# Kernel optimization log

Measured on AMD Instinct MI355X. Metric: run time of the kernel, lower is better.

Reference implementation:

```python
import jax, jax.numpy as jnp
import numpy as np

SIZES = jnp.array([128.0, 256.0, 512.0], dtype=jnp.float32)
RATIOS = jnp.array([0.5, 1.0, 2.0], dtype=jnp.float32)
SCORE_THR = 0.05
IOU_THR = 0.7
MIN_SIZE = 16.0
MAX_PROP = 1000
PRE_NMS = 1000


def _base_anchors():
    # torchvision-style base anchors: (x1,y1,x2,y2) centered at origin, rounded
    h_r = jnp.sqrt(RATIOS)
    w_r = 1.0 / h_r
    ws = (w_r[:, None] * SIZES[None, :]).reshape(-1)  # (9,)
    hs = (h_r[:, None] * SIZES[None, :]).reshape(-1)
    return jnp.round(jnp.stack([-ws, -hs, ws, hs], axis=1) / 2.0)  # (9,4)


def _grid_anchors(img_h, img_w, fh, fw):
    # stride = image_size // feature_size; anchors ordered (y, x, anchor)
    sh, sw = img_h // fh, img_w // fw
    sx = jnp.arange(fw, dtype=jnp.float32) * sw
    sy = jnp.arange(fh, dtype=jnp.float32) * sh
    yy, xx = jnp.meshgrid(sy, sx, indexing='ij')
    xf = xx.reshape(-1)
    yf = yy.reshape(-1)
    shifts = jnp.stack([xf, yf, xf, yf], axis=1)  # (H*W, 4)
    return (shifts[:, None, :] + _base_anchors()[None, :, :]).reshape(-1, 4)  # (H*W*9, 4)


def _conv(x, w, b, pad):
    y = jax.lax.conv_general_dilated(x, w, (1, 1), pad,
                                     dimension_numbers=('NCHW', 'OIHW', 'NCHW'))
    return y + b[None, :, None, None]


def _bbox_adjust(anchors, deltas):
    # anchors, deltas: (..., 4); deltas = (dx, dy, dw, dh)
    aw = anchors[..., 2] - anchors[..., 0]
    ah = anchors[..., 3] - anchors[..., 1]
    cx = anchors[..., 0] + 0.5 * aw
    cy = anchors[..., 1] + 0.5 * ah
    ncx = deltas[..., 0] * aw + cx
    ncy = deltas[..., 1] * ah + cy
    nw = jnp.exp(deltas[..., 2]) * aw
    nh = jnp.exp(deltas[..., 3]) * ah
    return jnp.stack([ncx - 0.5 * nw, ncy - 0.5 * nh,
                      ncx + 0.5 * nw, ncy + 0.5 * nh], axis=-1)


def _pairwise_iou(b):
    area = (b[:, 2] - b[:, 0]) * (b[:, 3] - b[:, 1])
    lt = jnp.maximum(b[:, None, :2], b[None, :, :2])
    rb = jnp.minimum(b[:, None, 2:], b[None, :, 2:])
    wh = jnp.clip(rb - lt, 0.0)
    inter = wh[..., 0] * wh[..., 1]
    return inter / (area[:, None] + area[None, :] - inter + 1e-8)


def _per_image(boxes, scores, img_h, img_w):
    # clip to image, filter small / low-score, greedy NMS, pad to MAX_PROP
    x1 = jnp.clip(boxes[:, 0], 0.0, img_w)
    y1 = jnp.clip(boxes[:, 1], 0.0, img_h)
    x2 = jnp.clip(boxes[:, 2], 0.0, img_w)
    y2 = jnp.clip(boxes[:, 3], 0.0, img_h)
    b = jnp.stack([x1, y1, x2, y2], axis=1)
    valid = ((x2 - x1) >= MIN_SIZE) & ((y2 - y1) >= MIN_SIZE) & (scores > SCORE_THR)
    s = jnp.where(valid, scores, -1.0)
    topv, topi = jax.lax.top_k(s, PRE_NMS)
    tb = b[topi]  # (PRE_NMS, 4) sorted by score desc
    iou = _pairwise_iou(tb)
    idx = jnp.arange(PRE_NMS)

    def body(i, keep):
        sup = (iou[i] > IOU_THR) & keep[i] & (idx > i)
        return keep & ~sup

    keep = jax.lax.fori_loop(0, PRE_NMS, body, jnp.ones(PRE_NMS, dtype=bool))
    s2 = jnp.where(keep & (topv > 0.0), topv, -1.0)
    fv, fi = jax.lax.top_k(s2, MAX_PROP)
    return jnp.where((fv > 0.0)[:, None], tb[fi], 0.0)  # (MAX_PROP, 4)


def _forward(image_list, feature_map, conv_w, conv_b, cls_w, cls_b, bbox_w, bbox_b):
    N, C, H, W = feature_map.shape
    img_h, img_w = image_list.shape[2], image_list.shape[3]
    out = _conv(feature_map, conv_w, conv_b, 'SAME')  # (N, mid, H, W)
    # faithful to original: cls reshaped directly (no permute), bbox permuted
    cls = jax.nn.sigmoid(_conv(out, cls_w, cls_b, 'VALID')).reshape(N, -1, 2)
    bb = _conv(out, bbox_w, bbox_b, 'VALID').transpose(0, 2, 3, 1).reshape(N, -1, 4)
    anchors = _grid_anchors(img_h, img_w, H, W)  # (H*W*9, 4)
    dec = _bbox_adjust(anchors[None], bb)        # (N, M, 4)
    scores = cls[:, :, 1]                        # objectness
    fh, fw = float(img_h), float(img_w)
    fb = jax.vmap(lambda bx, sc: _per_image(bx, sc, fh, fw))(dec, scores)  # (N, MAX_PROP, 4)
    roi = fb.reshape(-1, 4)
    bidx = jnp.repeat(jnp.arange(N, dtype=roi.dtype), MAX_PROP)[:, None]
    return jnp.concatenate([roi, bidx], axis=1)  # (N*MAX_PROP, 5)


def setup_inputs() -> dict:
    key = jax.random.key(0)
    ks = jax.random.split(key, 6)
    image_list = jax.random.normal(ks[0], (8, 3, 800, 800), dtype=jnp.float32)
    feature_map = jax.random.normal(ks[1], (8, 512, 50, 50), dtype=jnp.float32)
    conv_w = 0.02 * jax.random.normal(ks[2], (256, 512, 3, 3), dtype=jnp.float32)
    conv_b = jnp.zeros((256,), dtype=jnp.float32)
    cls_w = 0.02 * jax.random.normal(ks[3], (18, 256, 1, 1), dtype=jnp.float32)
    cls_b = jnp.zeros((18,), dtype=jnp.float32)
    bbox_w = 0.01 * jax.random.normal(ks[4], (36, 256, 1, 1), dtype=jnp.float32)
    bbox_b = jnp.zeros((36,), dtype=jnp.float32)
    return {"image_list": image_list, "feature_map": feature_map,
            "conv_w": conv_w, "conv_b": conv_b, "cls_w": cls_w, "cls_b": cls_b,
            "bbox_w": bbox_w, "bbox_b": bbox_b}


def reference(image_list, feature_map, conv_w, conv_b, cls_w, cls_b, bbox_w, bbox_b):
    return _forward(image_list, feature_map, conv_w, conv_b, cls_w, cls_b, bbox_w, bbox_b)
```

## Files before the change

### kernel.cpp

```cpp
#include <hip/hip_runtime.h>
#include <cstdint>

#define N_IMG 8
#define CIN 512
#define COUT 256
#define FH 50
#define FW 50
#define SPAT 2500
#define NANCH 22500
#define KTOP 1000
#define PART_ELEMS 5120000

__global__ __launch_bounds__(128) void k_conv3_part(const float* __restrict__ in,
                                                    const float* __restrict__ w,
                                                    double* __restrict__ parts)
{
    __shared__ double ind[2][672];

    const int tile = blockIdx.x, ocg = blockIdx.y;
    const int n = blockIdx.z >> 1, half = blockIdx.z & 1;
    const int cc0 = half << 5, cc1 = cc0 + 32;
    const int ty = tile / 5, tx = tile % 5;
    const int y0 = ty * 5, x0 = tx * 10;
    const int t = threadIdx.x;
    const int oc_l = t & 63;
    const int g = t >> 6;
    const int base_lx = g * 5;
    const int oc0 = ocg * 64;

    int soff[6];
#pragma unroll
    for (int k = 0; k < 6; k++) {
        int idx = t + k * 128;
        soff[k] = -1;
        if (idx < 672) {
            int c = idx / 84, rem = idx - c * 84;
            int iy = rem / 12, ix = rem - iy * 12;
            int y = y0 - 1 + iy, x = x0 - 1 + ix;
            if ((unsigned)y < 50u && (unsigned)x < 50u)
                soff[k] = (n * CIN + c) * SPAT + y * FW + x;
        }
    }

    const float* wrow = w + (size_t)(oc0 + oc_l) * (CIN * 9);

    double acc[5][5];
#pragma unroll
    for (int i = 0; i < 5; i++)
#pragma unroll
        for (int j = 0; j < 5; j++) acc[i][j] = 0.0;

    float rin[6];
    {
        const int coff0 = cc0 * (8 * SPAT);
#pragma unroll
        for (int k = 0; k < 6; k++) rin[k] = (soff[k] >= 0) ? in[soff[k] + coff0] : 0.0f;
    }
    float wnxt[9];
    {
        const float* wp0 = wrow + cc0 * 72;
#pragma unroll
        for (int k = 0; k < 9; k++) wnxt[k] = wp0[k];
    }

    for (int cc = cc0; cc < cc1; ++cc) {
        const int cur = cc & 1;
#pragma unroll
        for (int k = 0; k < 6; k++) {
            int idx = t + k * 128;
            if (idx < 672) ind[cur][idx] = (double)rin[k];
        }
        __syncthreads();

        if (cc + 1 < cc1) {
            const int coff = (cc + 1) * (8 * SPAT);
#pragma unroll
            for (int k = 0; k < 6; k++)
                rin[k] = (soff[k] >= 0) ? in[soff[k] + coff] : 0.0f;
        }

#pragma unroll 1
        for (int c = 0; c < 8; c++) {
            double wd[9];
#pragma unroll
            for (int k = 0; k < 9; k++) wd[k] = (double)wnxt[k];
            const int nidx = cc * 8 + c + 1;
            if (nidx < cc1 * 8) {
                const float* wp = wrow + nidx * 9;
#pragma unroll
                for (int k = 0; k < 9; k++) wnxt[k] = wp[k];
            }
#pragma unroll
            for (int r = 0; r < 7; r++) {
                double drow[7];
#pragma unroll
                for (int j = 0; j < 7; j++)
                    drow[j] = ind[cur][c * 84 + r * 12 + base_lx + j];
#pragma unroll
                for (int dy = 0; dy < 3; dy++) {
                    const int iy = r - dy;
                    if (iy >= 0 && iy < 5) {
#pragma unroll
                        for (int dx = 0; dx < 3; dx++) {
                            const double wdv = wd[dy * 3 + dx];
#pragma unroll
                            for (int ix = 0; ix < 5; ix++)
                                acc[iy][ix] = fma(wdv, drow[ix + dx], acc[iy][ix]);
                        }
                    }
                }
            }
        }
        __syncthreads();
    }

    double* po = parts + (size_t)half * PART_ELEMS + (size_t)(n * COUT + oc0 + oc_l) * SPAT;
#pragma unroll
    for (int iy = 0; iy < 5; iy++)
#pragma unroll
        for (int ix = 0; ix < 5; ix++)
            po[(y0 + iy) * FW + (x0 + base_lx + ix)] = acc[iy][ix];
}

__global__ __launch_bounds__(256) void k_combine(const double* __restrict__ parts,
                                                 const float* __restrict__ bias,
                                                 float* __restrict__ out)
{
    const int i = blockIdx.x * 256 + threadIdx.x;
    if (i < PART_ELEMS) {
        const int oc = (i / SPAT) & 255;
        out[i] = (float)(parts[i] + parts[i + PART_ELEMS] + (double)bias[oc]);
    }
}

__global__ __launch_bounds__(128) void k_conv3_full(const float* __restrict__ in,
                                                    const float* __restrict__ w,
                                                    const float* __restrict__ bias,
                                                    float* __restrict__ out)
{
    __shared__ double ind[2][672];

    const int tile = blockIdx.x, ocg = blockIdx.y, n = blockIdx.z;
    const int ty = tile / 5, tx = tile % 5;
    const int y0 = ty * 5, x0 = tx * 10;
    const int t = threadIdx.x;
    const int oc_l = t & 63;
    const int g = t >> 6;
    const int base_lx = g * 5;
    const int oc0 = ocg * 64;

    int soff[6];
#pragma unroll
    for (int k = 0; k < 6; k++) {
        int idx = t + k * 128;
        soff[k] = -1;
        if (idx < 672) {
            int c = idx / 84, rem = idx - c * 84;
            int iy = rem / 12, ix = rem - iy * 12;
            int y = y0 - 1 + iy, x = x0 - 1 + ix;
            if ((unsigned)y < 50u && (unsigned)x < 50u)
                soff[k] = (n * CIN + c) * SPAT + y * FW + x;
        }
    }

    const float* wrow = w + (size_t)(oc0 + oc_l) * (CIN * 9);

    double acc[5][5];
#pragma unroll
    for (int i = 0; i < 5; i++)
#pragma unroll
        for (int j = 0; j < 5; j++) acc[i][j] = 0.0;

    float rin[6];
#pragma unroll
    for (int k = 0; k < 6; k++) rin[k] = (soff[k] >= 0) ? in[soff[k]] : 0.0f;
    float wnxt[9];
#pragma unroll
    for (int k = 0; k < 9; k++) wnxt[k] = wrow[k];

    for (int cc = 0; cc < 64; ++cc) {
        const int cur = cc & 1;
#pragma unroll
        for (int k = 0; k < 6; k++) {
            int idx = t + k * 128;
            if (idx < 672) ind[cur][idx] = (double)rin[k];
        }
        __syncthreads();
        if (cc < 63) {
            const int coff = (cc + 1) * (8 * SPAT);
#pragma unroll
            for (int k = 0; k < 6; k++)
                rin[k] = (soff[k] >= 0) ? in[soff[k] + coff] : 0.0f;
        }
#pragma unroll 1
        for (int c = 0; c < 8; c++) {
            double wd[9];
#pragma unroll
            for (int k = 0; k < 9; k++) wd[k] = (double)wnxt[k];
            const int nidx = cc * 8 + c + 1;
            if (nidx < 512) {
                const float* wp = wrow + nidx * 9;
#pragma unroll
                for (int k = 0; k < 9; k++) wnxt[k] = wp[k];
            }
#pragma unroll
            for (int r = 0; r < 7; r++) {
                double drow[7];
#pragma unroll
                for (int j = 0; j < 7; j++)
                    drow[j] = ind[cur][c * 84 + r * 12 + base_lx + j];
#pragma unroll
                for (int dy = 0; dy < 3; dy++) {
                    const int iy = r - dy;
                    if (iy >= 0 && iy < 5) {
#pragma unroll
                        for (int dx = 0; dx < 3; dx++) {
                            const double wdv = wd[dy * 3 + dx];
#pragma unroll
                            for (int ix = 0; ix < 5; ix++)
                                acc[iy][ix] = fma(wdv, drow[ix + dx], acc[iy][ix]);
                        }
                    }
                }
            }
        }
        __syncthreads();
    }

    const double b = (double)bias[oc0 + oc_l];
#pragma unroll
    for (int iy = 0; iy < 5; iy++)
#pragma unroll
        for (int ix = 0; ix < 5; ix++) {
            int y = y0 + iy, x = x0 + base_lx + ix;
            out[(n * COUT + oc0 + oc_l) * SPAT + y * FW + x] = (float)(acc[iy][ix] + b);
        }
}

__global__ __launch_bounds__(256) void k_heads(const float* __restrict__ conv1,
                                               const float* __restrict__ cls_w,
                                               const float* __restrict__ cls_b,
                                               const float* __restrict__ bbox_w,
                                               const float* __restrict__ bbox_b,
                                               double* __restrict__ boxesd,
                                               double* __restrict__ scored)
{
    __shared__ float feat[25 * 257];
    __shared__ double outb[54 * 25];
    const int blk = blockIdx.x, n = blockIdx.y;
    const int pos0 = blk * 25;
    const int t = threadIdx.x;

    for (int idx = t; idx < 6400; idx += 256) {
        int c = idx / 25, p = idx - c * 25;
        feat[p * 257 + c] = conv1[(n * COUT + c) * SPAT + pos0 + p];
    }
    __syncthreads();

    for (int u = t; u < 1350; u += 256) {
        const int oc = u % 54, p = u / 54;
        const float* wp = (oc < 18) ? (cls_w + oc * COUT) : (bbox_w + (oc - 18) * COUT);
        double s = (double)((oc < 18) ? cls_b[oc] : bbox_b[oc - 18]);
        const float* fp = &feat[p * 257];
#pragma unroll 8
        for (int c = 0; c < COUT; c++) s = fma((double)wp[c], (double)fp[c], s);
        outb[oc * 25 + p] = s;
    }
    __syncthreads();

    if (t < 225) {
        const int p = t / 9, k = t - p * 9;
        const int pos = pos0 + p;
        const int y = pos / 50, x = pos - y * 50;
        const int ri = k / 3, si = k - ri * 3;
        const double ratio = (ri == 0) ? 0.5 : ((ri == 1) ? 1.0 : 2.0);
        const double size = (si == 0) ? 128.0 : ((si == 1) ? 256.0 : 512.0);
        const double hr = sqrt(ratio), wr = 1.0 / hr;
        const double wsz = wr * size, hsz = hr * size;
        const double bx0 = rint(-wsz * 0.5), by0 = rint(-hsz * 0.5);
        const double bx1 = rint(wsz * 0.5), by1 = rint(hsz * 0.5);
        const double sxf = (double)(x * 16), syf = (double)(y * 16);
        const double a0 = sxf + bx0, a1 = syf + by0, a2 = sxf + bx1, a3 = syf + by1;
        const double aw = a2 - a0, ah = a3 - a1;
        const double cx = a0 + 0.5 * aw, cy = a1 + 0.5 * ah;
        const double d0 = outb[(18 + k * 4 + 0) * 25 + p];
        const double d1 = outb[(18 + k * 4 + 1) * 25 + p];
        const double d2 = outb[(18 + k * 4 + 2) * 25 + p];
        const double d3 = outb[(18 + k * 4 + 3) * 25 + p];
        const double ncx = d0 * aw + cx, ncy = d1 * ah + cy;
        const double nw = exp(d2) * aw, nh = exp(d3) * ah;
        double x1 = ncx - 0.5 * nw, y1 = ncy - 0.5 * nh;
        double x2 = ncx + 0.5 * nw, y2 = ncy + 0.5 * nh;
        x1 = fmin(fmax(x1, 0.0), 800.0);
        y1 = fmin(fmax(y1, 0.0), 800.0);
        x2 = fmin(fmax(x2, 0.0), 800.0);
        y2 = fmin(fmax(y2, 0.0), 800.0);
        double* bp = boxesd + ((size_t)n * NANCH + pos * 9 + k) * 4;
        bp[0] = x1; bp[1] = y1; bp[2] = x2; bp[3] = y2;
    }
    for (int u = t; u < 450; u += 256) {
        const int ch = u / 25, p = u - ch * 25;
        const int pos = pos0 + p;
        if (pos & 1) {
            const int a = ch * 1250 + ((pos - 1) >> 1);
            const double v = outb[ch * 25 + p];
            scored[(size_t)n * NANCH + a] = 1.0 / (1.0 + exp(-v));
        }
    }
}

__global__ __launch_bounds__(1024) void k_select(const double* __restrict__ boxesd,
                                                 const double* __restrict__ scored,
                                                 uint64_t* __restrict__ keys,
                                                 double* __restrict__ tbd,
                                                 float* __restrict__ topv)
{
    __shared__ unsigned hist[256];
    __shared__ uint64_t selk[1024];
    __shared__ uint32_t seli[1024];
    __shared__ uint64_t sh_prefix, sh_mask;
    __shared__ unsigned sh_rem, sh_cntA, sh_cntB;

    const int n = blockIdx.x, t = threadIdx.x;
    uint64_t* ky = keys + (size_t)n * NANCH;

    for (int a = t; a < NANCH; a += 1024) {
        const double* bp = boxesd + ((size_t)n * NANCH + a) * 4;
        double x1 = bp[0], y1 = bp[1], x2 = bp[2], y2 = bp[3];
        double s0 = scored[(size_t)n * NANCH + a];
        bool valid = (x2 - x1 >= 16.0) && (y2 - y1 >= 16.0) && (s0 > 0.05);
        double s = valid ? s0 : -1.0;
        uint64_t b = (uint64_t)__double_as_longlong(s);
        uint64_t su = (b >> 63) ? ~b : (b | 0x8000000000000000ull);
        ky[a] = su;
    }
    if (t == 0) { sh_prefix = 0; sh_mask = 0; sh_rem = KTOP; }
    __syncthreads();

    for (int pass = 0; pass < 8; pass++) {
        const int shift = 56 - 8 * pass;
        if (t < 256) hist[t] = 0;
        __syncthreads();
        const uint64_t pre = sh_prefix, msk = sh_mask;
        for (int a = t; a < NANCH; a += 1024) {
            uint64_t k = ky[a];
            if ((k & msk) == pre)
                atomicAdd(&hist[(unsigned)((k >> shift) & 255)], 1u);
        }
        __syncthreads();
        if (t == 0) {
            unsigned rem = sh_rem;
            int v = 255;
            for (; v > 0; v--) {
                unsigned c = hist[v];
                if (rem <= c) break;
                rem -= c;
            }
            sh_prefix = pre | ((uint64_t)(unsigned)v << shift);
            sh_mask = msk | (255ull << shift);
            sh_rem = rem;
        }
        __syncthreads();
    }
    const uint64_t T = sh_prefix;
    selk[t] = 0; seli[t] = 0xFFFFFFFFu;
    if (t == 0) { sh_cntA = 0; sh_cntB = 0; }
    __syncthreads();
    for (int a = t; a < NANCH; a += 1024) {
        uint64_t k = ky[a];
        if (k > T) {
            unsigned p = atomicAdd(&sh_cntA, 1u);
            selk[p] = k; seli[p] = (uint32_t)a;
        }
    }
    __syncthreads();
    const unsigned m = sh_cntA;
    for (int a = t; a < NANCH; a += 1024) {
        uint64_t k = ky[a];
        if (k == T) {
            unsigned q = atomicAdd(&sh_cntB, 1u);
            unsigned slot = m + q;
            if (slot < KTOP) { selk[slot] = k; seli[slot] = (uint32_t)a; }
        }
    }
    __syncthreads();
    for (int k2 = 2; k2 <= 1024; k2 <<= 1) {
        for (int j = k2 >> 1; j > 0; j >>= 1) {
            int ixj = t ^ j;
            if (ixj > t) {
                bool asc = ((t & k2) == 0);
                uint64_t ka = selk[t], kb = selk[ixj];
                uint32_t ia = seli[t], ib = seli[ixj];
                bool gt = (ka > kb) || (ka == kb && ia < ib);
                if (gt == asc) { selk[t] = kb; selk[ixj] = ka; seli[t] = ib; seli[ixj] = ia; }
            }
            __syncthreads();
        }
    }
    if (t < KTOP) {
        uint64_t k = selk[1023 - t];
        uint32_t idx = seli[1023 - t];
        uint64_t b = (k >> 63) ? (k ^ 0x8000000000000000ull) : ~k;
        double s = __longlong_as_double((long long)b);
        const double* bp = boxesd + ((size_t)n * NANCH + idx) * 4;
        double* tp = tbd + ((size_t)n * KTOP + t) * 4;
        tp[0] = bp[0]; tp[1] = bp[1]; tp[2] = bp[2]; tp[3] = bp[3];
        topv[n * KTOP + t] = (float)s;
    }
}

__global__ __launch_bounds__(256) void k_supmat(const double* __restrict__ tbd,
                                                uint64_t* __restrict__ sup)
{
    __shared__ double sb[4000];
    const int tile = blockIdx.x, n = blockIdx.y;
    const int t = threadIdx.x;
    for (int i = t; i < 4000; i += 256) sb[i] = tbd[(size_t)n * KTOP * 4 + i];
    __syncthreads();
    const int r0 = tile * 64;
    for (int u = t; u < 1024; u += 256) {
        const int il = u >> 4, wq = u & 15;
        const int i = r0 + il;
        if (i >= 1000) continue;
        const double bix = sb[i * 4], biy = sb[i * 4 + 1], biz = sb[i * 4 + 2], biw = sb[i * 4 + 3];
        const double ai = (biz - bix) * (biw - biy);
        uint64_t bits = 0;
        const int jbase = wq * 64;
        for (int jj = 0; jj < 64; jj++) {
            const int j = jbase + jj;
            if (j < 1000 && j > i) {
                const double bjx = sb[j * 4], bjy = sb[j * 4 + 1], bjz = sb[j * 4 + 2], bjw = sb[j * 4 + 3];
                const double aj = (bjz - bjx) * (bjw - bjy);
                const double ltx = fmax(bix, bjx), lty = fmax(biy, bjy);
                const double rbx = fmin(biz, bjz), rby = fmin(biw, bjw);
                const double ww = fmax(rbx - ltx, 0.0), hh = fmax(rby - lty, 0.0);
                const double inter = ww * hh;
                const double iou = inter / (ai + aj - inter + 1e-8);
                if (iou > 0.7) bits |= (1ull << jj);
            }
        }
        sup[((size_t)n * KTOP + i) * 16 + wq] = bits;
    }
}

__global__ __launch_bounds__(64) void k_nms(const uint64_t* __restrict__ sup,
                                            uint64_t* __restrict__ keepout)
{
    const int n = blockIdx.x;
    const int lane = threadIdx.x;
    const uint64_t* rows = sup + (size_t)n * KTOP * 16;

    uint64_t keep;
    if (lane < 15) keep = ~0ull;
    else if (lane == 15) keep = (1ull << 40) - 1;
    else keep = 0;

    uint64_t A[8], B[8];
    auto LOADG = [&](uint64_t* dst, int g) {
#pragma unroll
        for (int k = 0; k < 8; k++) {
            int i = g * 8 + k;
            dst[k] = (lane < 16) ? rows[(size_t)i * 16 + lane] : 0ull;
        }
    };
    auto PROCG = [&](const uint64_t* src, int g) {
#pragma unroll
        for (int k = 0; k < 8; k++) {
            int i = g * 8 + k;
            uint64_t kw = __shfl(keep, i >> 6);
            bool alive = (kw >> (i & 63)) & 1ull;
            keep &= alive ? ~src[k] : ~0ull;
        }
    };

    LOADG(A, 0);
    for (int g = 0; g < 125; g += 2) {
        if (g + 1 < 125) LOADG(B, g + 1);
        PROCG(A, g);
        if (g + 2 < 125) LOADG(A, g + 2);
        if (g + 1 < 125) PROCG(B, g + 1);
    }
    if (lane < 16) keepout[n * 16 + lane] = keep;
}

__global__ __launch_bounds__(1024) void k_final(const uint64_t* __restrict__ keepw,
                                                const float* __restrict__ topv,
                                                const double* __restrict__ tbd,
                                                float* __restrict__ out)
{
    __shared__ int sc[1024];
    __shared__ uint64_t kw[16];
    __shared__ int sh_total;
    const int n = blockIdx.x, t = threadIdx.x;
    if (t < 16) kw[t] = keepw[n * 16 + t];
    __syncthreads();

    int val = 0;
    bool kept = false;
    if (t < 1000) {
        bool bit = (kw[t >> 6] >> (t & 63)) & 1ull;
        float v = topv[n * KTOP + t];
        kept = bit && (v > 0.0f);
        val = kept ? 1 : 0;
    }
    sc[t] = val;
    __syncthreads();
    for (int off = 1; off < 1024; off <<= 1) {
        int x = (t >= off) ? sc[t - off] : 0;
        __syncthreads();
        sc[t] += x;
        __syncthreads();
    }
    if (t == 1023) sh_total = sc[1023];
    __syncthreads();
    const int total = sh_total;
    if (t < 1000) {
        if (kept) {
            int r = sc[t] - 1;
            const double* bp = tbd + ((size_t)n * KTOP + t) * 4;
            float* o = out + ((size_t)n * KTOP + r) * 5;
            o[0] = (float)bp[0]; o[1] = (float)bp[1];
            o[2] = (float)bp[2]; o[3] = (float)bp[3];
            o[4] = (float)n;
        }
        if (t >= total) {
            float* o = out + ((size_t)n * KTOP + t) * 5;
            o[0] = 0.0f; o[1] = 0.0f; o[2] = 0.0f; o[3] = 0.0f; o[4] = (float)n;
        }
    }
}

extern "C" void kernel_launch(void* const* d_in, const int* in_sizes, int n_in,
                              void* d_out, int out_size, void* d_ws, size_t ws_size,
                              hipStream_t stream)
{
    (void)in_sizes; (void)n_in; (void)out_size;
    const float* feat   = (const float*)d_in[1];
    const float* conv_w = (const float*)d_in[2];
    const float* conv_b = (const float*)d_in[3];
    const float* cls_w  = (const float*)d_in[4];
    const float* cls_b  = (const float*)d_in[5];
    const float* bbox_w = (const float*)d_in[6];
    const float* bbox_b = (const float*)d_in[7];
    float* out = (float*)d_out;
    char* ws = (char*)d_ws;

    const size_t NEED_SPLIT = 2ull * 40960000 + 20480000 + 5760000 + 1440000
                            + 1440000 + 256000 + 32000 + 1024000 + 1024;

    if (ws_size >= NEED_SPLIT) {
        double*   parts  = (double*)(ws);
        float*    conv1  = (float*)(ws + 81920000);
        double*   boxesd = (double*)(ws + 102400000);
        double*   scored = (double*)(ws + 108160000);
        uint64_t* keys   = (uint64_t*)(ws + 109600000);
        double*   tbd    = (double*)(ws + 111040000);
        float*    topv   = (float*)(ws + 111296000);
        uint64_t* sup    = (uint64_t*)(ws + 111328000);
        uint64_t* keepw  = (uint64_t*)(ws + 112352000);

        k_conv3_part<<<dim3(50, 4, 16), 128, 0, stream>>>(feat, conv_w, parts);
        k_combine   <<<(PART_ELEMS + 255) / 256, 256, 0, stream>>>(parts, conv_b, conv1);
        k_heads <<<dim3(100, 8),   256, 0, stream>>>(conv1, cls_w, cls_b, bbox_w, bbox_b, boxesd, scored);
        k_select<<<8, 1024, 0, stream>>>(boxesd, scored, keys, tbd, topv);
        k_supmat<<<dim3(16, 8), 256, 0, stream>>>(tbd, sup);
        k_nms   <<<8, 64, 0, stream>>>(sup, keepw);
        k_final <<<8, 1024, 0, stream>>>(keepw, topv, tbd, out);
    } else {
        float*    conv1  = (float*)(ws);
        double*   boxesd = (double*)(ws + 20480000);
        double*   scored = (double*)(ws + 26240000);
        uint64_t* keys   = (uint64_t*)(ws + 27680000);
        double*   tbd    = (double*)(ws + 29120000);
        float*    topv   = (float*)(ws + 29376000);
        uint64_t* sup    = (uint64_t*)(ws + 29408000);
        uint64_t* keepw  = (uint64_t*)(ws + 30432000);

        k_conv3_full<<<dim3(50, 4, 8), 128, 0, stream>>>(feat, conv_w, conv_b, conv1);
        k_heads <<<dim3(100, 8),   256, 0, stream>>>(conv1, cls_w, cls_b, bbox_w, bbox_b, boxesd, scored);
        k_select<<<8, 1024, 0, stream>>>(boxesd, scored, keys, tbd, topv);
        k_supmat<<<dim3(16, 8), 256, 0, stream>>>(tbd, sup);
        k_nms   <<<8, 64, 0, stream>>>(sup, keepw);
        k_final <<<8, 1024, 0, stream>>>(keepw, topv, tbd, out);
    }
}
```

Measured before the change: 1.583 ms.

## Enlarge conv tiles, add variable channel split, fuse partial sum into heads

The 3x3 conv kernel now uses 256-thread blocks covering 10x10 spatial tiles, so each staged input patch in shared memory is reused by four position groups instead of two. The input-channel split count S (4, 2 or 1) is picked from the available workspace rather than fixed at 2. The separate combine kernel is removed: the heads kernel sums the S partial buffers and adds the conv bias while loading features, which saves a float intermediate round trip and one launch. With S=4 the partial buffers get larger and the heads kernel reads more double data, and fewer channels per block means relatively more setup and store cost.

```diff
diff --git a/kernel.cpp b/kernel.cpp
--- a/kernel.cpp
+++ b/kernel.cpp
@@ -11,30 +11,32 @@
 #define KTOP 1000
 #define PART_ELEMS 5120000
 
-__global__ __launch_bounds__(128) void k_conv3_part(const float* __restrict__ in,
+__global__ __launch_bounds__(256) void k_conv3_part(const float* __restrict__ in,
                                                     const float* __restrict__ w,
-                                                    double* __restrict__ parts)
-{
-    __shared__ double ind[2][672];
+                                                    double* __restrict__ parts,
+                                                    int S)
+{
+    __shared__ double ind[2][1152];
 
     const int tile = blockIdx.x, ocg = blockIdx.y;
-    const int n = blockIdx.z >> 1, half = blockIdx.z & 1;
-    const int cc0 = half << 5, cc1 = cc0 + 32;
+    const int n = blockIdx.z / S, s = blockIdx.z - n * S;
+    const int ccp = 64 / S;
+    const int cc0 = s * ccp, cc1 = cc0 + ccp;
     const int ty = tile / 5, tx = tile % 5;
-    const int y0 = ty * 5, x0 = tx * 10;
+    const int y0 = ty * 10, x0 = tx * 10;
     const int t = threadIdx.x;
     const int oc_l = t & 63;
     const int g = t >> 6;
-    const int base_lx = g * 5;
+    const int base_ly = (g >> 1) * 5, base_lx = (g & 1) * 5;
     const int oc0 = ocg * 64;
 
-    int soff[6];
-#pragma unroll
-    for (int k = 0; k < 6; k++) {
-        int idx = t + k * 128;
+    int soff[5];
+#pragma unroll
+    for (int k = 0; k < 5; k++) {
+        int idx = t + k * 256;
         soff[k] = -1;
-        if (idx < 672) {
-            int c = idx / 84, rem = idx - c * 84;
+        if (idx < 1152) {
+            int c = idx / 144, rem = idx - c * 144;
             int iy = rem / 12, ix = rem - iy * 12;
             int y = y0 - 1 + iy, x = x0 - 1 + ix;
             if ((unsigned)y < 50u && (unsigned)x < 50u)
@@ -50,11 +52,11 @@
 #pragma unroll
         for (int j = 0; j < 5; j++) acc[i][j] = 0.0;
 
-    float rin[6];
+    float rin[5];
     {
         const int coff0 = cc0 * (8 * SPAT);
 #pragma unroll
-        for (int k = 0; k < 6; k++) rin[k] = (soff[k] >= 0) ? in[soff[k] + coff0] : 0.0f;
+        for (int k = 0; k < 5; k++) rin[k] = (soff[k] >= 0) ? in[soff[k] + coff0] : 0.0f;
     }
     float wnxt[9];
     {
@@ -66,16 +68,16 @@
     for (int cc = cc0; cc < cc1; ++cc) {
         const int cur = cc & 1;
 #pragma unroll
-        for (int k = 0; k < 6; k++) {
-            int idx = t + k * 128;
-            if (idx < 672) ind[cur][idx] = (double)rin[k];
+        for (int k = 0; k < 5; k++) {
+            int idx = t + k * 256;
+            if (idx < 1152) ind[cur][idx] = (double)rin[k];
         }
         __syncthreads();
 
         if (cc + 1 < cc1) {
             const int coff = (cc + 1) * (8 * SPAT);
 #pragma unroll
-            for (int k = 0; k < 6; k++)
+            for (int k = 0; k < 5; k++)
                 rin[k] = (soff[k] >= 0) ? in[soff[k] + coff] : 0.0f;
         }
 
@@ -95,7 +97,7 @@
                 double drow[7];
 #pragma unroll
                 for (int j = 0; j < 7; j++)
-                    drow[j] = ind[cur][c * 84 + r * 12 + base_lx + j];
+                    drow[j] = ind[cur][c * 144 + (base_ly + r) * 12 + base_lx + j];
 #pragma unroll
                 for (int dy = 0; dy < 3; dy++) {
                     const int iy = r - dy;
@@ -114,136 +116,23 @@
         __syncthreads();
     }
 
-    double* po = parts + (size_t)half * PART_ELEMS + (size_t)(n * COUT + oc0 + oc_l) * SPAT;
+    double* po = parts + (size_t)s * PART_ELEMS + (size_t)(n * COUT + oc0 + oc_l) * SPAT;
 #pragma unroll
     for (int iy = 0; iy < 5; iy++)
 #pragma unroll
         for (int ix = 0; ix < 5; ix++)
-            po[(y0 + iy) * FW + (x0 + base_lx + ix)] = acc[iy][ix];
-}
-
-__global__ __launch_bounds__(256) void k_combine(const double* __restrict__ parts,
-                                                 const float* __restrict__ bias,
-                                                 float* __restrict__ out)
-{
-    const int i = blockIdx.x * 256 + threadIdx.x;
-    if (i < PART_ELEMS) {
-        const int oc = (i / SPAT) & 255;
-        out[i] = (float)(parts[i] + parts[i + PART_ELEMS] + (double)bias[oc]);
-    }
-}
-
-__global__ __launch_bounds__(128) void k_conv3_full(const float* __restrict__ in,
-                                                    const float* __restrict__ w,
-                                                    const float* __restrict__ bias,
-                                                    float* __restrict__ out)
-{
-    __shared__ double ind[2][672];
-
-    const int tile = blockIdx.x, ocg = blockIdx.y, n = blockIdx.z;
-    const int ty = tile / 5, tx = tile % 5;
-    const int y0 = ty * 5, x0 = tx * 10;
-    const int t = threadIdx.x;
-    const int oc_l = t & 63;
-    const int g = t >> 6;
-    const int base_lx = g * 5;
-    const int oc0 = ocg * 64;
-
-    int soff[6];
-#pragma unroll
-    for (int k = 0; k < 6; k++) {
-        int idx = t + k * 128;
-        soff[k] = -1;
-        if (idx < 672) {
-            int c = idx / 84, rem = idx - c * 84;
-            int iy = rem / 12, ix = rem - iy * 12;
-            int y = y0 - 1 + iy, x = x0 - 1 + ix;
-            if ((unsigned)y < 50u && (unsigned)x < 50u)
-                soff[k] = (n * CIN + c) * SPAT + y * FW + x;
-        }
-    }
-
-    const float* wrow = w + (size_t)(oc0 + oc_l) * (CIN * 9);
-
-    double acc[5][5];
-#pragma unroll
-    for (int i = 0; i < 5; i++)
-#pragma unroll
-        for (int j = 0; j < 5; j++) acc[i][j] = 0.0;
-
-    float rin[6];
-#pragma unroll
-    for (int k = 0; k < 6; k++) rin[k] = (soff[k] >= 0) ? in[soff[k]] : 0.0f;
-    float wnxt[9];
-#pragma unroll
-    for (int k = 0; k < 9; k++) wnxt[k] = wrow[k];
-
-    for (int cc = 0; cc < 64; ++cc) {
-        const int cur = cc & 1;
-#pragma unroll
-        for (int k = 0; k < 6; k++) {
-            int idx = t + k * 128;
-            if (idx < 672) ind[cur][idx] = (double)rin[k];
-        }
-        __syncthreads();
-        if (cc < 63) {
-            const int coff = (cc + 1) * (8 * SPAT);
-#pragma unroll
-            for (int k = 0; k < 6; k++)
-                rin[k] = (soff[k] >= 0) ? in[soff[k] + coff] : 0.0f;
-        }
-#pragma unroll 1
-        for (int c = 0; c < 8; c++) {
-            double wd[9];
-#pragma unroll
-            for (int k = 0; k < 9; k++) wd[k] = (double)wnxt[k];
-            const int nidx = cc * 8 + c + 1;
-            if (nidx < 512) {
-                const float* wp = wrow + nidx * 9;
-#pragma unroll
-                for (int k = 0; k < 9; k++) wnxt[k] = wp[k];
-            }
-#pragma unroll
-            for (int r = 0; r < 7; r++) {
-                double drow[7];
-#pragma unroll
-                for (int j = 0; j < 7; j++)
-                    drow[j] = ind[cur][c * 84 + r * 12 + base_lx + j];
-#pragma unroll
-                for (int dy = 0; dy < 3; dy++) {
-                    const int iy = r - dy;
-                    if (iy >= 0 && iy < 5) {
-#pragma unroll
-                        for (int dx = 0; dx < 3; dx++) {
-                            const double wdv = wd[dy * 3 + dx];
-#pragma unroll
-                            for (int ix = 0; ix < 5; ix++)
-                                acc[iy][ix] = fma(wdv, drow[ix + dx], acc[iy][ix]);
-                        }
-                    }
-                }
-            }
-        }
-        __syncthreads();
-    }
-
-    const double b = (double)bias[oc0 + oc_l];
-#pragma unroll
-    for (int iy = 0; iy < 5; iy++)
-#pragma unroll
-        for (int ix = 0; ix < 5; ix++) {
-            int y = y0 + iy, x = x0 + base_lx + ix;
-            out[(n * COUT + oc0 + oc_l) * SPAT + y * FW + x] = (float)(acc[iy][ix] + b);
-        }
-}
-
-__global__ __launch_bounds__(256) void k_heads(const float* __restrict__ conv1,
-                                               const float* __restrict__ cls_w,
-                                               const float* __restrict__ cls_b,
-                                               const float* __restrict__ bbox_w,
-                                               const float* __restrict__ bbox_b,
-                                               double* __restrict__ boxesd,
-                                               double* __restrict__ scored)
+            po[(y0 + base_ly + iy) * FW + (x0 + base_lx + ix)] = acc[iy][ix];
+}
+
+__global__ __launch_bounds__(256) void k_heads_fused(const double* __restrict__ parts,
+                                                     int S,
+                                                     const float* __restrict__ conv_b,
+                                                     const float* __restrict__ cls_w,
+                                                     const float* __restrict__ cls_b,
+                                                     const float* __restrict__ bbox_w,
+                                                     const float* __restrict__ bbox_b,
+                                                     double* __restrict__ boxesd,
+                                                     double* __restrict__ scored)
 {
     __shared__ float feat[25 * 257];
     __shared__ double outb[54 * 25];
@@ -253,7 +142,11 @@
 
     for (int idx = t; idx < 6400; idx += 256) {
         int c = idx / 25, p = idx - c * 25;
-        feat[p * 257 + c] = conv1[(n * COUT + c) * SPAT + pos0 + p];
+        size_t base = (size_t)(n * COUT + c) * SPAT + pos0 + p;
+        double a = parts[base];
+        for (int sp = 1; sp < S; sp++) a += parts[(size_t)sp * PART_ELEMS + base];
+        a += (double)conv_b[c];
+        feat[p * 257 + c] = (float)a;
     }
     __syncthreads();
 
@@ -309,6 +202,175 @@
     }
 }
 
+__global__ __launch_bounds__(128) void k_conv3_full(const float* __restrict__ in,
+                                                    const float* __restrict__ w,
+                                                    const float* __restrict__ bias,
+                                                    float* __restrict__ out)
+{
+    __shared__ double ind[2][672];
+    const int tile = blockIdx.x, ocg = blockIdx.y, n = blockIdx.z;
+    const int ty = tile / 5, tx = tile % 5;
+    const int y0 = ty * 5, x0 = tx * 10;
+    const int t = threadIdx.x;
+    const int oc_l = t & 63;
+    const int g = t >> 6;
+    const int base_lx = g * 5;
+    const int oc0 = ocg * 64;
+
+    int soff[6];
+#pragma unroll
+    for (int k = 0; k < 6; k++) {
+        int idx = t + k * 128;
+        soff[k] = -1;
+        if (idx < 672) {
+            int c = idx / 84, rem = idx - c * 84;
+            int iy = rem / 12, ix = rem - iy * 12;
+            int y = y0 - 1 + iy, x = x0 - 1 + ix;
+            if ((unsigned)y < 50u && (unsigned)x < 50u)
+                soff[k] = (n * CIN + c) * SPAT + y * FW + x;
+        }
+    }
+    const float* wrow = w + (size_t)(oc0 + oc_l) * (CIN * 9);
+    double acc[5][5];
+#pragma unroll
+    for (int i = 0; i < 5; i++)
+#pragma unroll
+        for (int j = 0; j < 5; j++) acc[i][j] = 0.0;
+    float rin[6];
+#pragma unroll
+    for (int k = 0; k < 6; k++) rin[k] = (soff[k] >= 0) ? in[soff[k]] : 0.0f;
+    float wnxt[9];
+#pragma unroll
+    for (int k = 0; k < 9; k++) wnxt[k] = wrow[k];
+
+    for (int cc = 0; cc < 64; ++cc) {
+        const int cur = cc & 1;
+#pragma unroll
+        for (int k = 0; k < 6; k++) {
+            int idx = t + k * 128;
+            if (idx < 672) ind[cur][idx] = (double)rin[k];
+        }
+        __syncthreads();
+        if (cc < 63) {
+            const int coff = (cc + 1) * (8 * SPAT);
+#pragma unroll
+            for (int k = 0; k < 6; k++)
+                rin[k] = (soff[k] >= 0) ? in[soff[k] + coff] : 0.0f;
+        }
+#pragma unroll 1
+        for (int c = 0; c < 8; c++) {
+            double wd[9];
+#pragma unroll
+            for (int k = 0; k < 9; k++) wd[k] = (double)wnxt[k];
+            const int nidx = cc * 8 + c + 1;
+            if (nidx < 512) {
+                const float* wp = wrow + nidx * 9;
+#pragma unroll
+                for (int k = 0; k < 9; k++) wnxt[k] = wp[k];
+            }
+#pragma unroll
+            for (int r = 0; r < 7; r++) {
+                double drow[7];
+#pragma unroll
+                for (int j = 0; j < 7; j++)
+                    drow[j] = ind[cur][c * 84 + r * 12 + base_lx + j];
+#pragma unroll
+                for (int dy = 0; dy < 3; dy++) {
+                    const int iy = r - dy;
+                    if (iy >= 0 && iy < 5) {
+#pragma unroll
+                        for (int dx = 0; dx < 3; dx++) {
+                            const double wdv = wd[dy * 3 + dx];
+#pragma unroll
+                            for (int ix = 0; ix < 5; ix++)
+                                acc[iy][ix] = fma(wdv, drow[ix + dx], acc[iy][ix]);
+                        }
+                    }
+                }
+            }
+        }
+        __syncthreads();
+    }
+    const double b = (double)bias[oc0 + oc_l];
+#pragma unroll
+    for (int iy = 0; iy < 5; iy++)
+#pragma unroll
+        for (int ix = 0; ix < 5; ix++) {
+            int y = y0 + iy, x = x0 + base_lx + ix;
+            out[(n * COUT + oc0 + oc_l) * SPAT + y * FW + x] = (float)(acc[iy][ix] + b);
+        }
+}
+
+__global__ __launch_bounds__(256) void k_heads_legacy(const float* __restrict__ conv1,
+                                                      const float* __restrict__ cls_w,
+                                                      const float* __restrict__ cls_b,
+                                                      const float* __restrict__ bbox_w,
+                                                      const float* __restrict__ bbox_b,
+                                                      double* __restrict__ boxesd,
+                                                      double* __restrict__ scored)
+{
+    __shared__ float feat[25 * 257];
+    __shared__ double outb[54 * 25];
+    const int blk = blockIdx.x, n = blockIdx.y;
+    const int pos0 = blk * 25;
+    const int t = threadIdx.x;
+
+    for (int idx = t; idx < 6400; idx += 256) {
+        int c = idx / 25, p = idx - c * 25;
+        feat[p * 257 + c] = conv1[(n * COUT + c) * SPAT + pos0 + p];
+    }
+    __syncthreads();
+    for (int u = t; u < 1350; u += 256) {
+        const int oc = u % 54, p = u / 54;
+        const float* wp = (oc < 18) ? (cls_w + oc * COUT) : (bbox_w + (oc - 18) * COUT);
+        double s = (double)((oc < 18) ? cls_b[oc] : bbox_b[oc - 18]);
+        const float* fp = &feat[p * 257];
+#pragma unroll 8
+        for (int c = 0; c < COUT; c++) s = fma((double)wp[c], (double)fp[c], s);
+        outb[oc * 25 + p] = s;
+    }
+    __syncthreads();
+    if (t < 225) {
+        const int p = t / 9, k = t - p * 9;
+        const int pos = pos0 + p;
+        const int y = pos / 50, x = pos - y * 50;
+        const int ri = k / 3, si = k - ri * 3;
+        const double ratio = (ri == 0) ? 0.5 : ((ri == 1) ? 1.0 : 2.0);
+        const double size = (si == 0) ? 128.0 : ((si == 1) ? 256.0 : 512.0);
+        const double hr = sqrt(ratio), wr = 1.0 / hr;
+        const double wsz = wr * size, hsz = hr * size;
+        const double bx0 = rint(-wsz * 0.5), by0 = rint(-hsz * 0.5);
+        const double bx1 = rint(wsz * 0.5), by1 = rint(hsz * 0.5);
+        const double sxf = (double)(x * 16), syf = (double)(y * 16);
+        const double a0 = sxf + bx0, a1 = syf + by0, a2 = sxf + bx1, a3 = syf + by1;
+        const double aw = a2 - a0, ah = a3 - a1;
+        const double cx = a0 + 0.5 * aw, cy = a1 + 0.5 * ah;
+        const double d0 = outb[(18 + k * 4 + 0) * 25 + p];
+        const double d1 = outb[(18 + k * 4 + 1) * 25 + p];
+        const double d2 = outb[(18 + k * 4 + 2) * 25 + p];
+        const double d3 = outb[(18 + k * 4 + 3) * 25 + p];
+        const double ncx = d0 * aw + cx, ncy = d1 * ah + cy;
+        const double nw = exp(d2) * aw, nh = exp(d3) * ah;
+        double x1 = ncx - 0.5 * nw, y1 = ncy - 0.5 * nh;
+        double x2 = ncx + 0.5 * nw, y2 = ncy + 0.5 * nh;
+        x1 = fmin(fmax(x1, 0.0), 800.0);
+        y1 = fmin(fmax(y1, 0.0), 800.0);
+        x2 = fmin(fmax(x2, 0.0), 800.0);
+        y2 = fmin(fmax(y2, 0.0), 800.0);
+        double* bp = boxesd + ((size_t)n * NANCH + pos * 9 + k) * 4;
+        bp[0] = x1; bp[1] = y1; bp[2] = x2; bp[3] = y2;
+    }
+    for (int u = t; u < 450; u += 256) {
+        const int ch = u / 25, p = u - ch * 25;
+        const int pos = pos0 + p;
+        if (pos & 1) {
+            const int a = ch * 1250 + ((pos - 1) >> 1);
+            const double v = outb[ch * 25 + p];
+            scored[(size_t)n * NANCH + a] = 1.0 / (1.0 + exp(-v));
+        }
+    }
+}
+
 __global__ __launch_bounds__(1024) void k_select(const double* __restrict__ boxesd,
                                                  const double* __restrict__ scored,
                                                  uint64_t* __restrict__ keys,
@@ -545,23 +607,28 @@
     float* out = (float*)d_out;
     char* ws = (char*)d_ws;
 
-    const size_t NEED_SPLIT = 2ull * 40960000 + 20480000 + 5760000 + 1440000
-                            + 1440000 + 256000 + 32000 + 1024000 + 1024;
-
-    if (ws_size >= NEED_SPLIT) {
-        double*   parts  = (double*)(ws);
-        float*    conv1  = (float*)(ws + 81920000);
-        double*   boxesd = (double*)(ws + 102400000);
-        double*   scored = (double*)(ws + 108160000);
-        uint64_t* keys   = (uint64_t*)(ws + 109600000);
-        double*   tbd    = (double*)(ws + 111040000);
-        float*    topv   = (float*)(ws + 111296000);
-        uint64_t* sup    = (uint64_t*)(ws + 111328000);
-        uint64_t* keepw  = (uint64_t*)(ws + 112352000);
-
-        k_conv3_part<<<dim3(50, 4, 16), 128, 0, stream>>>(feat, conv_w, parts);
-        k_combine   <<<(PART_ELEMS + 255) / 256, 256, 0, stream>>>(parts, conv_b, conv1);
-        k_heads <<<dim3(100, 8),   256, 0, stream>>>(conv1, cls_w, cls_b, bbox_w, bbox_b, boxesd, scored);
+    const size_t PB   = 40960000ull;
+    const size_t REST = 5760000 + 1440000 + 1440000 + 256000 + 32000 + 1024000 + 1024;
+
+    int S = 0;
+    if      (ws_size >= 4 * PB + REST) S = 4;
+    else if (ws_size >= 2 * PB + REST) S = 2;
+    else if (ws_size >= 1 * PB + REST) S = 1;
+
+    if (S > 0) {
+        double*   parts  = (double*)ws;
+        char*     p      = ws + (size_t)S * PB;
+        double*   boxesd = (double*)(p);               p += 5760000;
+        double*   scored = (double*)(p);               p += 1440000;
+        uint64_t* keys   = (uint64_t*)(p);             p += 1440000;
+        double*   tbd    = (double*)(p);               p += 256000;
+        float*    topv   = (float*)(p);                p += 32000;
+        uint64_t* sup    = (uint64_t*)(p);             p += 1024000;
+        uint64_t* keepw  = (uint64_t*)(p);
+
+        k_conv3_part <<<dim3(25, 4, 8 * S), 256, 0, stream>>>(feat, conv_w, parts, S);
+        k_heads_fused<<<dim3(100, 8), 256, 0, stream>>>(parts, S, conv_b, cls_w, cls_b,
+                                                        bbox_w, bbox_b, boxesd, scored);
         k_select<<<8, 1024, 0, stream>>>(boxesd, scored, keys, tbd, topv);
         k_supmat<<<dim3(16, 8), 256, 0, stream>>>(tbd, sup);
         k_nms   <<<8, 64, 0, stream>>>(sup, keepw);
@@ -576,8 +643,8 @@
         uint64_t* sup    = (uint64_t*)(ws + 29408000);
         uint64_t* keepw  = (uint64_t*)(ws + 30432000);
 
-        k_conv3_full<<<dim3(50, 4, 8), 128, 0, stream>>>(feat, conv_w, conv_b, conv1);
-        k_heads <<<dim3(100, 8),   256, 0, stream>>>(conv1, cls_w, cls_b, bbox_w, bbox_b, boxesd, scored);
+        k_conv3_full  <<<dim3(50, 4, 8), 128, 0, stream>>>(feat, conv_w, conv_b, conv1);
+        k_heads_legacy<<<dim3(100, 8), 256, 0, stream>>>(conv1, cls_w, cls_b, bbox_w, bbox_b, boxesd, scored);
         k_select<<<8, 1024, 0, stream>>>(boxesd, scored, keys, tbd, topv);
         k_supmat<<<dim3(16, 8), 256, 0, stream>>>(tbd, sup);
         k_nms   <<<8, 64, 0, stream>>>(sup, keepw);
```

After: 1.500 ms. -5.3%, faster.
